# Kernel optimization log

Hardware: AMD Instinct MI355X
Metric: run time of the kernel (lower is better)

Reference implementation:

```python
import jax, jax.numpy as jnp
import numpy as np
from jax import lax

EPS = 1e-9

def _squash(v):
    # v: [..., D]; squash nonlinearity from CapsNet
    n = jnp.sum(jnp.square(v), axis=-1, keepdims=True)
    return (n / (1.0 + n) / jnp.sqrt(n + EPS)) * v

def setup_inputs() -> dict:
    key = jax.random.key(0)
    ks = jax.random.split(key, 12)
    B, S, D, NI = 1024, 200, 64, 4
    N_UID, N_MID = 50000, 100000
    return {
        "uid": jax.random.randint(ks[0], (B,), 0, N_UID, dtype=jnp.int32),
        "age": jax.random.randint(ks[1], (B,), 0, N_UID, dtype=jnp.int32),
        "gender": jax.random.randint(ks[2], (B,), 0, N_UID, dtype=jnp.int32),
        "occup": jax.random.randint(ks[3], (B,), 0, N_UID, dtype=jnp.int32),
        "mid_his": jax.random.randint(ks[4], (B, S), 0, N_MID, dtype=jnp.int32),
        "mask": jax.random.randint(ks[5], (B, S), 0, 2).astype(jnp.float32),
        "user_emb_table": jax.random.normal(ks[6], (N_UID, D), jnp.float32) * 0.1,
        "age_table": jax.random.normal(ks[7], (N_UID, D), jnp.float32) * 0.1,
        "gender_table": jax.random.normal(ks[8], (N_UID, D), jnp.float32) * 0.1,
        "occup_table": jax.random.normal(ks[9], (N_UID, D), jnp.float32) * 0.1,
        "mid_emb_table": jax.random.normal(ks[10], (N_MID, D), jnp.float32) * 0.1,
        "w_capsule": jax.random.normal(ks[11], (S, NI * D, D), jnp.float32),
    }

def reference(uid, age, gender, occup, mid_his, mask,
              user_emb_table, age_table, gender_table, occup_table,
              mid_emb_table, w_capsule):
    NI = 4
    B, S = mid_his.shape
    D = mid_emb_table.shape[1]

    # user profile: mean of 4 stacked user feature embeddings
    user_profile = (user_emb_table[uid] + gender_table[gender]
                    + age_table[age] + occup_table[occup]) * 0.25  # [B,D]

    # masked item history embeddings
    item_his = mid_emb_table[mid_his] * mask[:, :, None]  # [B,S,D]

    # adjacency: sigmoid(sum_d h_i[d]*h_j[d]*u[d]) without [B,S,S,D] blowup
    hu = item_his * user_profile[:, None, :]              # [B,S,D]
    adj = jax.nn.sigmoid(jnp.einsum('bid,bjd->bij', hu, item_his))  # [B,S,S]
    adj = adj * mask[:, None, :] * mask[:, :, None]

    # --- CapsuleNetwork, bilinear_type=2 ---
    # TF: sum(w[1,S,NI*D,D] * u[B,S,1,D], axis=3) == contraction over D
    hat = jnp.einsum('bsd,sed->bse', item_his, w_capsule)  # [B,S,NI*D]
    hat = hat.reshape(B, S, NI, D).transpose(0, 2, 1, 3)   # [B,NI,S,D]
    hat_iter = lax.stop_gradient(hat)

    cw = jnp.zeros((B, NI, S), dtype=item_his.dtype)  # routing logits
    atten_mask = mask[:, None, :]                     # [B,1,S] broadcast over NI
    for i in range(3):
        sw = jax.nn.softmax(cw, axis=1)               # softmax over interests
        sw = jnp.where(atten_mask == 0, 0.0, sw)      # [B,NI,S]
        if i < 2:
            cap = _squash(jnp.einsum('bks,bksd->bkd', sw, hat_iter))  # [B,NI,D]
            delta = jnp.einsum('bksd,bkd->bks', hat_iter, cap)
            cw = cw + delta
        else:
            cap = _squash(jnp.einsum('bks,bksd->bkd', sw, hat))
    interest_capsule = cap  # [B,NI,D]; relu_layer=False -> no projection
    return interest_capsule, adj
```

## Files before the change

### kernel.cpp

```cpp
#include <hip/hip_runtime.h>

#define B_SZ 1024
#define S_SZ 200
#define D_SZ 64
#define NI_SZ 4
#define E_SZ 256

using u16 = unsigned short;
using u32 = unsigned int;
typedef short  sh8    __attribute__((ext_vector_type(8)));
typedef __bf16 bf16x8 __attribute__((ext_vector_type(8)));
typedef float  f32x4  __attribute__((ext_vector_type(4)));

__device__ __forceinline__ u16 f2bf(float x) {
  u32 u = __float_as_uint(x);
  u += 0x7FFFu + ((u >> 16) & 1u);
  return (u16)(u >> 16);
}
__device__ __forceinline__ float bf2f(u16 h) {
  return __uint_as_float(((u32)h) << 16);
}
__device__ __forceinline__ sh8 ldsr(const u16* arr, int row, int kshort) {
  const int idx = row * 64 + (kshort ^ ((row & 7) << 3));
  return *(const sh8*)(arr + idx);
}
__device__ __forceinline__ bf16x8 ldsw(const u16* arr, int row, int kshort) {
  return __builtin_bit_cast(bf16x8, ldsr(arr, row, kshort));
}
__device__ __forceinline__ void stsw(u16* arr, int row, int c, sh8 v) {
  *(sh8*)(arr + row * 64 + 8 * (c ^ (row & 7))) = v;
}

__global__ __launch_bounds__(256) void wconv_kernel(
    const float* __restrict__ W, u16* __restrict__ Wb)
{
  const int idx = blockIdx.x * 256 + threadIdx.x;
  if (idx >= S_SZ * E_SZ * D_SZ / 8) return;
  const float4 a = *(const float4*)(W + (size_t)idx * 8);
  const float4 b = *(const float4*)(W + (size_t)idx * 8 + 4);
  sh8 r;
  r[0] = (short)f2bf(a.x); r[1] = (short)f2bf(a.y);
  r[2] = (short)f2bf(a.z); r[3] = (short)f2bf(a.w);
  r[4] = (short)f2bf(b.x); r[5] = (short)f2bf(b.y);
  r[6] = (short)f2bf(b.z); r[7] = (short)f2bf(b.w);
  *(sh8*)(Wb + (size_t)idx * 8) = r;
}

__global__ __launch_bounds__(256, 4) void adj_fused(
    const int* __restrict__ uid, const int* __restrict__ age,
    const int* __restrict__ gender, const int* __restrict__ occup,
    const float* __restrict__ U, const float* __restrict__ AT,
    const float* __restrict__ GT, const float* __restrict__ OT,
    const int* __restrict__ mid_his, const float* __restrict__ mask,
    const float* __restrict__ memb,
    u16* __restrict__ item_bs, float* __restrict__ adj)
{
  const int b = blockIdx.x;
  __shared__ u16   Hs[208 * 64];
  __shared__ float Ms[208];
  __shared__ int   midS[S_SZ];
  __shared__ float pS[D_SZ];
  const int tid = threadIdx.x;

  if (tid < 208) Ms[tid] = (tid < S_SZ) ? mask[b * S_SZ + tid] : 0.f;
  if (tid < S_SZ) midS[tid] = mid_his[b * S_SZ + tid];
  if (tid < D_SZ) {
    float v = U[(size_t)uid[b]    * D_SZ + tid]
            + GT[(size_t)gender[b] * D_SZ + tid]
            + AT[(size_t)age[b]    * D_SZ + tid]
            + OT[(size_t)occup[b]  * D_SZ + tid];
    pS[tid] = 0.25f * v;
  }
  __syncthreads();

  for (int idx = tid; idx < S_SZ * 8; idx += 256) {
    const int row = idx >> 3, c = idx & 7;
    const float m = Ms[row];
    const float* src = memb + (size_t)midS[row] * D_SZ + c * 8;
    const float4 a = *(const float4*)(src);
    const float4 d = *(const float4*)(src + 4);
    sh8 v;
    v[0] = (short)f2bf(a.x * m); v[1] = (short)f2bf(a.y * m);
    v[2] = (short)f2bf(a.z * m); v[3] = (short)f2bf(a.w * m);
    v[4] = (short)f2bf(d.x * m); v[5] = (short)f2bf(d.y * m);
    v[6] = (short)f2bf(d.z * m); v[7] = (short)f2bf(d.w * m);
    stsw(Hs, row, c, v);
    *(sh8*)(item_bs + ((size_t)b * S_SZ + row) * D_SZ + c * 8) = v;
  }
  if (tid < 64) {
    sh8 z = {0,0,0,0,0,0,0,0};
    stsw(Hs, S_SZ + (tid >> 3), tid & 7, z);
  }
  __syncthreads();

  const int w = tid >> 6, l = tid & 63;
  const int lr = l & 15, lg = l >> 4;
  float pvA[8], pvB[8];
  #pragma unroll
  for (int j = 0; j < 8; j++) { pvA[j] = pS[lg * 8 + j]; pvB[j] = pS[32 + lg * 8 + j]; }

  float* outb = adj + (size_t)b * S_SZ * S_SZ;
  for (int mt = 0; mt < 13; mt++) {
    const int arow = mt * 16 + lr;
    const sh8 r0 = ldsr(Hs, arow, lg * 8);
    const sh8 r1 = ldsr(Hs, arow, 32 + lg * 8);
    sh8 h0, h1;
    #pragma unroll
    for (int j = 0; j < 8; j++) {
      h0[j] = (short)f2bf(bf2f((u16)r0[j]) * pvA[j]);
      h1[j] = (short)f2bf(bf2f((u16)r1[j]) * pvB[j]);
    }
    const bf16x8 a0 = __builtin_bit_cast(bf16x8, h0);
    const bf16x8 a1 = __builtin_bit_cast(bf16x8, h1);
    for (int nt = w; nt < 13; nt += 4) {
      const int brow = nt * 16 + lr;
      const bf16x8 b0 = ldsw(Hs, brow, lg * 8);
      const bf16x8 b1 = ldsw(Hs, brow, 32 + lg * 8);
      f32x4 acc = {0.f, 0.f, 0.f, 0.f};
      acc = __builtin_amdgcn_mfma_f32_16x16x32_bf16(a0, b0, acc, 0, 0, 0);
      acc = __builtin_amdgcn_mfma_f32_16x16x32_bf16(a1, b1, acc, 0, 0, 0);
      const int n = nt * 16 + lr;
      const float mj = Ms[n];
      #pragma unroll
      for (int r = 0; r < 4; r++) {
        const int m = mt * 16 + lg * 4 + r;
        if (m < S_SZ && n < S_SZ) {
          const float sg = 1.f / (1.f + __expf(-acc[r]));
          outb[(size_t)m * S_SZ + n] = sg * Ms[m] * mj;
        }
      }
    }
  }
}

__global__ __launch_bounds__(256, 4) void hat_mfma(
    const u16* __restrict__ item_bs, const u16* __restrict__ Wb,
    u16* __restrict__ hatb)
{
  const int s  = blockIdx.y;
  const int b0 = blockIdx.x * 64;
  __shared__ u16 As[64 * 64];
  __shared__ u16 Ws_[256 * 64];
  const int tid = threadIdx.x;

  for (int idx = tid; idx < 64 * 8; idx += 256) {
    const int row = idx >> 3, c = idx & 7;
    const sh8 v = *(const sh8*)(item_bs + ((size_t)(b0 + row) * S_SZ + s) * D_SZ + c * 8);
    stsw(As, row, c, v);
  }
  for (int idx = tid; idx < 256 * 8; idx += 256) {
    const int row = idx >> 3, c = idx & 7;
    const sh8 v = *(const sh8*)(Wb + ((size_t)s * E_SZ + row) * D_SZ + c * 8);
    stsw(Ws_, row, c, v);
  }
  __syncthreads();

  const int w = tid >> 6, l = tid & 63;
  const int lr = l & 15, lg = l >> 4;

  f32x4 acc[4][4];
  #pragma unroll
  for (int mt = 0; mt < 4; mt++)
    #pragma unroll
    for (int nt = 0; nt < 4; nt++) acc[mt][nt] = (f32x4){0.f, 0.f, 0.f, 0.f};

  #pragma unroll
  for (int ks = 0; ks < 2; ks++) {
    bf16x8 af[4], bf_[4];
    #pragma unroll
    for (int mt = 0; mt < 4; mt++)
      af[mt] = ldsw(As, mt * 16 + lr, ks * 32 + lg * 8);
    #pragma unroll
    for (int nt = 0; nt < 4; nt++)
      bf_[nt] = ldsw(Ws_, w * 64 + nt * 16 + lr, ks * 32 + lg * 8);
    #pragma unroll
    for (int mt = 0; mt < 4; mt++)
      #pragma unroll
      for (int nt = 0; nt < 4; nt++)
        acc[mt][nt] = __builtin_amdgcn_mfma_f32_16x16x32_bf16(af[mt], bf_[nt], acc[mt][nt], 0, 0, 0);
  }

  #pragma unroll
  for (int mt = 0; mt < 4; mt++) {
    #pragma unroll
    for (int r = 0; r < 4; r++) {
      const int bb = b0 + mt * 16 + lg * 4 + r;
      u16* dst = hatb + (((size_t)bb * NI_SZ + w) * S_SZ + s) * D_SZ;
      #pragma unroll
      for (int nt = 0; nt < 4; nt++)
        dst[nt * 16 + lr] = f2bf(acc[mt][nt][r]);
    }
  }
}

__device__ __forceinline__ float rlane(float v, int l) {
  return __int_as_float(__builtin_amdgcn_readlane(__float_as_int(v), l));
}

__global__ __launch_bounds__(1024, 4) void route_kernel(
    const u16* __restrict__ hatb, const float* __restrict__ mask,
    float* __restrict__ out)
{
  const int b = blockIdx.x;
  const int t = threadIdx.x;
  const int w = t >> 6, lane = t & 63;
  const int k = w >> 2, q = w & 3;
  __shared__ float cwS[NI_SZ][212];
  __shared__ float partS[NI_SZ][4][D_SZ];

  const float msv = (lane < 50) ? mask[b * S_SZ + q * 50 + lane] : 0.f;

  float hr[50];
  const u16* hg = hatb + (((size_t)b * NI_SZ + k) * S_SZ + q * 50) * D_SZ + lane;
  #pragma unroll
  for (int j = 0; j < 50; j++) hr[j] = bf2f(hg[j * D_SZ]);
  #pragma unroll
  for (int j = 0; j < 50; j++) asm volatile("" : "+v"(hr[j]));

  const int jj = __brev(lane) >> 26;

  for (int iter = 0; iter < 3; ++iter) {
    float swv;
    if (iter == 0) {
      swv = 0.25f * msv;
    } else {
      const int sidx = q * 50 + (lane < 50 ? lane : 49);
      const float a0 = cwS[0][sidx], a1 = cwS[1][sidx],
                  a2 = cwS[2][sidx], a3 = cwS[3][sidx];
      const float mx = fmaxf(fmaxf(a0, a1), fmaxf(a2, a3));
      const float e0 = __expf(a0 - mx), e1 = __expf(a1 - mx),
                  e2 = __expf(a2 - mx), e3 = __expf(a3 - mx);
      const float ek = (k == 0) ? e0 : (k == 1) ? e1 : (k == 2) ? e2 : e3;
      const float inv = 1.f / (e0 + e1 + e2 + e3);
      swv = (msv == 0.f) ? 0.f : ek * inv;
    }

    float c0 = 0.f, c1 = 0.f, c2 = 0.f, c3 = 0.f;
    #pragma unroll
    for (int j = 0; j < 48; j += 4) {
      c0 = fmaf(rlane(swv, j + 0), hr[j + 0], c0);
      c1 = fmaf(rlane(swv, j + 1), hr[j + 1], c1);
      c2 = fmaf(rlane(swv, j + 2), hr[j + 2], c2);
      c3 = fmaf(rlane(swv, j + 3), hr[j + 3], c3);
    }
    c0 = fmaf(rlane(swv, 48), hr[48], c0);
    c1 = fmaf(rlane(swv, 49), hr[49], c1);
    partS[k][q][lane] = (c0 + c2) + (c1 + c3);
    __syncthreads();

    const float cap = partS[k][0][lane] + partS[k][1][lane]
                    + partS[k][2][lane] + partS[k][3][lane];
    float n = cap * cap;
    #pragma unroll
    for (int off = 32; off; off >>= 1) n += __shfl_xor(n, off);
    const float f = n / (1.f + n) * rsqrtf(n + 1e-9f);
    const float capd = cap * f;

    if (iter < 2) {
      float p[32];
      {
        const int bit = lane & 1;
        #pragma unroll
        for (int j = 0; j < 32; j++) {
          const float lo = hr[j] * capd;
          const float hi = (j + 32 < 50) ? hr[j + 32] * capd : 0.f;
          const float send = bit ? lo : hi;
          const float keep = bit ? hi : lo;
          p[j] = keep + __shfl_xor(send, 1);
        }
      }
      #pragma unroll
      for (int r = 1; r < 6; r++) {
        const int dist = 1 << r;
        const int half = 32 >> r;
        const int bit = (lane >> r) & 1;
        #pragma unroll
        for (int j = 0; j < 32; j++) {
          if (j < half) {
            const float send = bit ? p[j] : p[j + half];
            const float keep = bit ? p[j + half] : p[j];
            p[j] = keep + __shfl_xor(send, dist);
          }
        }
      }
      if (jj < 50) {
        if (iter == 0) cwS[k][q * 50 + jj] = p[0];
        else           cwS[k][q * 50 + jj] += p[0];
      }
      __syncthreads();
    } else if (q == 0) {
      out[((size_t)b * NI_SZ + k) * D_SZ + lane] = capd;
    }
  }
}

extern "C" void kernel_launch(void* const* d_in, const int* in_sizes, int n_in,
                              void* d_out, int out_size, void* d_ws, size_t ws_size,
                              hipStream_t stream)
{
  const int*   uid     = (const int*)d_in[0];
  const int*   age     = (const int*)d_in[1];
  const int*   gender  = (const int*)d_in[2];
  const int*   occup   = (const int*)d_in[3];
  const int*   mid_his = (const int*)d_in[4];
  const float* mask    = (const float*)d_in[5];
  const float* U       = (const float*)d_in[6];
  const float* AT      = (const float*)d_in[7];
  const float* GT      = (const float*)d_in[8];
  const float* OT      = (const float*)d_in[9];
  const float* ME      = (const float*)d_in[10];
  const float* WC      = (const float*)d_in[11];

  float* out  = (float*)d_out;
  float* adj  = out + B_SZ * NI_SZ * D_SZ;

  char* ws = (char*)d_ws;
  u16*   item_bs = (u16*)ws;
  u16*   Wb      = (u16*)(ws + 26214400);
  u16*   hatb    = (u16*)(ws + 26214400 + 6553600);

  wconv_kernel<<<(S_SZ * E_SZ * D_SZ / 8 + 255) / 256, 256, 0, stream>>>(WC, Wb);
  adj_fused<<<B_SZ, 256, 0, stream>>>(uid, age, gender, occup, U, AT, GT, OT,
                                      mid_his, mask, ME, item_bs, adj);
  hat_mfma<<<dim3(16, S_SZ), 256, 0, stream>>>(item_bs, Wb, hatb);
  route_kernel<<<B_SZ, 1024, 0, stream>>>(hatb, mask, out);
}
```

Measured before the change: 169.7 us.

## Merge adj, weight conversion and hat GEMM into one interleaved heterogeneous kernel

Replaces three launches (weight fp32→bf16 conversion, adjacency kernel, hat GEMM) with a single kernel whose blocks are split into adjacency blocks and hat-GEMM blocks, interleaved 8:25 per group. The hat blocks now gather item embeddings and convert W directly from fp32, so the item_bs and Wb workspace round trips and two launch boundaries go away. The cost is redundant fp32 W loads and conversions (each W slice is read by 16 blocks) and redundant embedding gathers, and the two work types must share one launch configuration and one shared-memory size.

Result: slower. 177.6 us (+4.6%).

```diff
diff --git a/kernel.cpp b/kernel.cpp
--- a/kernel.cpp
+++ b/kernel.cpp
@@ -30,165 +30,151 @@
 __device__ __forceinline__ void stsw(u16* arr, int row, int c, sh8 v) {
   *(sh8*)(arr + row * 64 + 8 * (c ^ (row & 7))) = v;
 }
-
-__global__ __launch_bounds__(256) void wconv_kernel(
-    const float* __restrict__ W, u16* __restrict__ Wb)
-{
-  const int idx = blockIdx.x * 256 + threadIdx.x;
-  if (idx >= S_SZ * E_SZ * D_SZ / 8) return;
-  const float4 a = *(const float4*)(W + (size_t)idx * 8);
-  const float4 b = *(const float4*)(W + (size_t)idx * 8 + 4);
-  sh8 r;
-  r[0] = (short)f2bf(a.x); r[1] = (short)f2bf(a.y);
-  r[2] = (short)f2bf(a.z); r[3] = (short)f2bf(a.w);
-  r[4] = (short)f2bf(b.x); r[5] = (short)f2bf(b.y);
-  r[6] = (short)f2bf(b.z); r[7] = (short)f2bf(b.w);
-  *(sh8*)(Wb + (size_t)idx * 8) = r;
-}
-
-__global__ __launch_bounds__(256, 4) void adj_fused(
+__device__ __forceinline__ sh8 cvt8(const float* __restrict__ src, float m) {
+  const float4 a = *(const float4*)(src);
+  const float4 d = *(const float4*)(src + 4);
+  sh8 v;
+  v[0] = (short)f2bf(a.x * m); v[1] = (short)f2bf(a.y * m);
+  v[2] = (short)f2bf(a.z * m); v[3] = (short)f2bf(a.w * m);
+  v[4] = (short)f2bf(d.x * m); v[5] = (short)f2bf(d.y * m);
+  v[6] = (short)f2bf(d.z * m); v[7] = (short)f2bf(d.w * m);
+  return v;
+}
+
+__global__ __launch_bounds__(256, 4) void mega_kernel(
     const int* __restrict__ uid, const int* __restrict__ age,
     const int* __restrict__ gender, const int* __restrict__ occup,
     const float* __restrict__ U, const float* __restrict__ AT,
     const float* __restrict__ GT, const float* __restrict__ OT,
     const int* __restrict__ mid_his, const float* __restrict__ mask,
-    const float* __restrict__ memb,
-    u16* __restrict__ item_bs, float* __restrict__ adj)
+    const float* __restrict__ memb, const float* __restrict__ WC,
+    float* __restrict__ adj, u16* __restrict__ hatb)
 {
-  const int b = blockIdx.x;
-  __shared__ u16   Hs[208 * 64];
-  __shared__ float Ms[208];
-  __shared__ int   midS[S_SZ];
-  __shared__ float pS[D_SZ];
+  __shared__ __align__(16) char smem[40960];
   const int tid = threadIdx.x;
-
-  if (tid < 208) Ms[tid] = (tid < S_SZ) ? mask[b * S_SZ + tid] : 0.f;
-  if (tid < S_SZ) midS[tid] = mid_his[b * S_SZ + tid];
-  if (tid < D_SZ) {
-    float v = U[(size_t)uid[b]    * D_SZ + tid]
-            + GT[(size_t)gender[b] * D_SZ + tid]
-            + AT[(size_t)age[b]    * D_SZ + tid]
-            + OT[(size_t)occup[b]  * D_SZ + tid];
-    pS[tid] = 0.25f * v;
-  }
-  __syncthreads();
-
-  for (int idx = tid; idx < S_SZ * 8; idx += 256) {
-    const int row = idx >> 3, c = idx & 7;
-    const float m = Ms[row];
-    const float* src = memb + (size_t)midS[row] * D_SZ + c * 8;
-    const float4 a = *(const float4*)(src);
-    const float4 d = *(const float4*)(src + 4);
-    sh8 v;
-    v[0] = (short)f2bf(a.x * m); v[1] = (short)f2bf(a.y * m);
-    v[2] = (short)f2bf(a.z * m); v[3] = (short)f2bf(a.w * m);
-    v[4] = (short)f2bf(d.x * m); v[5] = (short)f2bf(d.y * m);
-    v[6] = (short)f2bf(d.z * m); v[7] = (short)f2bf(d.w * m);
-    stsw(Hs, row, c, v);
-    *(sh8*)(item_bs + ((size_t)b * S_SZ + row) * D_SZ + c * 8) = v;
-  }
-  if (tid < 64) {
-    sh8 z = {0,0,0,0,0,0,0,0};
-    stsw(Hs, S_SZ + (tid >> 3), tid & 7, z);
-  }
-  __syncthreads();
-
-  const int w = tid >> 6, l = tid & 63;
-  const int lr = l & 15, lg = l >> 4;
-  float pvA[8], pvB[8];
-  #pragma unroll
-  for (int j = 0; j < 8; j++) { pvA[j] = pS[lg * 8 + j]; pvB[j] = pS[32 + lg * 8 + j]; }
-
-  float* outb = adj + (size_t)b * S_SZ * S_SZ;
-  for (int mt = 0; mt < 13; mt++) {
-    const int arow = mt * 16 + lr;
-    const sh8 r0 = ldsr(Hs, arow, lg * 8);
-    const sh8 r1 = ldsr(Hs, arow, 32 + lg * 8);
-    sh8 h0, h1;
-    #pragma unroll
-    for (int j = 0; j < 8; j++) {
-      h0[j] = (short)f2bf(bf2f((u16)r0[j]) * pvA[j]);
-      h1[j] = (short)f2bf(bf2f((u16)r1[j]) * pvB[j]);
-    }
-    const bf16x8 a0 = __builtin_bit_cast(bf16x8, h0);
-    const bf16x8 a1 = __builtin_bit_cast(bf16x8, h1);
-    for (int nt = w; nt < 13; nt += 4) {
-      const int brow = nt * 16 + lr;
-      const bf16x8 b0 = ldsw(Hs, brow, lg * 8);
-      const bf16x8 b1 = ldsw(Hs, brow, 32 + lg * 8);
-      f32x4 acc = {0.f, 0.f, 0.f, 0.f};
-      acc = __builtin_amdgcn_mfma_f32_16x16x32_bf16(a0, b0, acc, 0, 0, 0);
-      acc = __builtin_amdgcn_mfma_f32_16x16x32_bf16(a1, b1, acc, 0, 0, 0);
-      const int n = nt * 16 + lr;
-      const float mj = Ms[n];
-      #pragma unroll
-      for (int r = 0; r < 4; r++) {
-        const int m = mt * 16 + lg * 4 + r;
-        if (m < S_SZ && n < S_SZ) {
-          const float sg = 1.f / (1.f + __expf(-acc[r]));
-          outb[(size_t)m * S_SZ + n] = sg * Ms[m] * mj;
+  const int g = blockIdx.x / 33, r = blockIdx.x % 33;
+
+  if (r < 8) {
+    const int b = g * 8 + r;
+    u16*   Hs   = (u16*)smem;
+    float* Ms   = (float*)(smem + 26624);
+    int*   midS = (int*)(smem + 27456);
+    float* pS   = (float*)(smem + 28256);
+
+    if (tid < 208) Ms[tid] = (tid < S_SZ) ? mask[b * S_SZ + tid] : 0.f;
+    if (tid < S_SZ) midS[tid] = mid_his[b * S_SZ + tid];
+    if (tid < D_SZ) {
+      float v = U[(size_t)uid[b]     * D_SZ + tid]
+              + GT[(size_t)gender[b] * D_SZ + tid]
+              + AT[(size_t)age[b]    * D_SZ + tid]
+              + OT[(size_t)occup[b]  * D_SZ + tid];
+      pS[tid] = 0.25f * v;
+    }
+    __syncthreads();
+
+    for (int idx = tid; idx < S_SZ * 8; idx += 256) {
+      const int row = idx >> 3, c = idx & 7;
+      stsw(Hs, row, c, cvt8(memb + (size_t)midS[row] * D_SZ + c * 8, Ms[row]));
+    }
+    if (tid < 64) {
+      sh8 z = {0,0,0,0,0,0,0,0};
+      stsw(Hs, S_SZ + (tid >> 3), tid & 7, z);
+    }
+    __syncthreads();
+
+    const int w = tid >> 6, l = tid & 63;
+    const int lr = l & 15, lg = l >> 4;
+    float pvA[8], pvB[8];
+    #pragma unroll
+    for (int j = 0; j < 8; j++) { pvA[j] = pS[lg * 8 + j]; pvB[j] = pS[32 + lg * 8 + j]; }
+
+    float* outb = adj + (size_t)b * S_SZ * S_SZ;
+    for (int mt = 0; mt < 13; mt++) {
+      const int arow = mt * 16 + lr;
+      const sh8 r0 = ldsr(Hs, arow, lg * 8);
+      const sh8 r1 = ldsr(Hs, arow, 32 + lg * 8);
+      sh8 h0, h1;
+      #pragma unroll
+      for (int j = 0; j < 8; j++) {
+        h0[j] = (short)f2bf(bf2f((u16)r0[j]) * pvA[j]);
+        h1[j] = (short)f2bf(bf2f((u16)r1[j]) * pvB[j]);
+      }
+      const bf16x8 a0 = __builtin_bit_cast(bf16x8, h0);
+      const bf16x8 a1 = __builtin_bit_cast(bf16x8, h1);
+      for (int nt = w; nt < 13; nt += 4) {
+        const int brow = nt * 16 + lr;
+        const bf16x8 b0 = ldsw(Hs, brow, lg * 8);
+        const bf16x8 b1 = ldsw(Hs, brow, 32 + lg * 8);
+        f32x4 acc = {0.f, 0.f, 0.f, 0.f};
+        acc = __builtin_amdgcn_mfma_f32_16x16x32_bf16(a0, b0, acc, 0, 0, 0);
+        acc = __builtin_amdgcn_mfma_f32_16x16x32_bf16(a1, b1, acc, 0, 0, 0);
+        const int n = nt * 16 + lr;
+        const float mj = Ms[n];
+        #pragma unroll
+        for (int rr = 0; rr < 4; rr++) {
+          const int m = mt * 16 + lg * 4 + rr;
+          if (m < S_SZ && n < S_SZ) {
+            const float sg = 1.f / (1.f + __expf(-acc[rr]));
+            outb[(size_t)m * S_SZ + n] = sg * Ms[m] * mj;
+          }
         }
       }
     }
-  }
-}
-
-__global__ __launch_bounds__(256, 4) void hat_mfma(
-    const u16* __restrict__ item_bs, const u16* __restrict__ Wb,
-    u16* __restrict__ hatb)
-{
-  const int s  = blockIdx.y;
-  const int b0 = blockIdx.x * 64;
-  __shared__ u16 As[64 * 64];
-  __shared__ u16 Ws_[256 * 64];
-  const int tid = threadIdx.x;
-
-  for (int idx = tid; idx < 64 * 8; idx += 256) {
-    const int row = idx >> 3, c = idx & 7;
-    const sh8 v = *(const sh8*)(item_bs + ((size_t)(b0 + row) * S_SZ + s) * D_SZ + c * 8);
-    stsw(As, row, c, v);
-  }
-  for (int idx = tid; idx < 256 * 8; idx += 256) {
-    const int row = idx >> 3, c = idx & 7;
-    const sh8 v = *(const sh8*)(Wb + ((size_t)s * E_SZ + row) * D_SZ + c * 8);
-    stsw(Ws_, row, c, v);
-  }
-  __syncthreads();
-
-  const int w = tid >> 6, l = tid & 63;
-  const int lr = l & 15, lg = l >> 4;
-
-  f32x4 acc[4][4];
-  #pragma unroll
-  for (int mt = 0; mt < 4; mt++)
-    #pragma unroll
-    for (int nt = 0; nt < 4; nt++) acc[mt][nt] = (f32x4){0.f, 0.f, 0.f, 0.f};
-
-  #pragma unroll
-  for (int ks = 0; ks < 2; ks++) {
-    bf16x8 af[4], bf_[4];
+  } else {
+    const int hi = g * 25 + (r - 8);
+    const int s  = hi >> 4;
+    const int b0 = (hi & 15) * 64;
+    u16* As  = (u16*)smem;
+    u16* Ws_ = (u16*)(smem + 8192);
+
+    for (int idx = tid; idx < 64 * 8; idx += 256) {
+      const int row = idx >> 3, c = idx & 7;
+      const int bb = b0 + row;
+      const int mid = mid_his[bb * S_SZ + s];
+      const float m = mask[bb * S_SZ + s];
+      stsw(As, row, c, cvt8(memb + (size_t)mid * D_SZ + c * 8, m));
+    }
+    for (int idx = tid; idx < 256 * 8; idx += 256) {
+      const int row = idx >> 3, c = idx & 7;
+      stsw(Ws_, row, c, cvt8(WC + ((size_t)s * E_SZ + row) * D_SZ + c * 8, 1.f));
+    }
+    __syncthreads();
+
+    const int w = tid >> 6, l = tid & 63;
+    const int lr = l & 15, lg = l >> 4;
+
+    f32x4 acc[4][4];
     #pragma unroll
     for (int mt = 0; mt < 4; mt++)
-      af[mt] = ldsw(As, mt * 16 + lr, ks * 32 + lg * 8);
-    #pragma unroll
-    for (int nt = 0; nt < 4; nt++)
-      bf_[nt] = ldsw(Ws_, w * 64 + nt * 16 + lr, ks * 32 + lg * 8);
-    #pragma unroll
-    for (int mt = 0; mt < 4; mt++)
+      #pragma unroll
+      for (int nt = 0; nt < 4; nt++) acc[mt][nt] = (f32x4){0.f, 0.f, 0.f, 0.f};
+
+    #pragma unroll
+    for (int ks = 0; ks < 2; ks++) {
+      bf16x8 af[4], bf_[4];
+      #pragma unroll
+      for (int mt = 0; mt < 4; mt++)
+        af[mt] = ldsw(As, mt * 16 + lr, ks * 32 + lg * 8);
       #pragma unroll
       for (int nt = 0; nt < 4; nt++)
-        acc[mt][nt] = __builtin_amdgcn_mfma_f32_16x16x32_bf16(af[mt], bf_[nt], acc[mt][nt], 0, 0, 0);
-  }
-
-  #pragma unroll
-  for (int mt = 0; mt < 4; mt++) {
-    #pragma unroll
-    for (int r = 0; r < 4; r++) {
-      const int bb = b0 + mt * 16 + lg * 4 + r;
-      u16* dst = hatb + (((size_t)bb * NI_SZ + w) * S_SZ + s) * D_SZ;
-      #pragma unroll
-      for (int nt = 0; nt < 4; nt++)
-        dst[nt * 16 + lr] = f2bf(acc[mt][nt][r]);
+        bf_[nt] = ldsw(Ws_, w * 64 + nt * 16 + lr, ks * 32 + lg * 8);
+      #pragma unroll
+      for (int mt = 0; mt < 4; mt++)
+        #pragma unroll
+        for (int nt = 0; nt < 4; nt++)
+          acc[mt][nt] = __builtin_amdgcn_mfma_f32_16x16x32_bf16(af[mt], bf_[nt], acc[mt][nt], 0, 0, 0);
+    }
+
+    #pragma unroll
+    for (int mt = 0; mt < 4; mt++) {
+      #pragma unroll
+      for (int rr = 0; rr < 4; rr++) {
+        const int bb = b0 + mt * 16 + lg * 4 + rr;
+        u16* dst = hatb + (((size_t)bb * NI_SZ + w) * S_SZ + s) * D_SZ;
+        #pragma unroll
+        for (int nt = 0; nt < 4; nt++)
+          dst[nt * 16 + lr] = f2bf(acc[mt][nt][rr]);
+      }
     }
   }
 }
@@ -270,10 +256,10 @@
         }
       }
       #pragma unroll
-      for (int r = 1; r < 6; r++) {
-        const int dist = 1 << r;
-        const int half = 32 >> r;
-        const int bit = (lane >> r) & 1;
+      for (int rr = 1; rr < 6; rr++) {
+        const int dist = 1 << rr;
+        const int half = 32 >> rr;
+        const int bit = (lane >> rr) & 1;
         #pragma unroll
         for (int j = 0; j < 32; j++) {
           if (j < half) {
@@ -314,14 +300,9 @@
   float* out  = (float*)d_out;
   float* adj  = out + B_SZ * NI_SZ * D_SZ;
 
-  char* ws = (char*)d_ws;
-  u16*   item_bs = (u16*)ws;
-  u16*   Wb      = (u16*)(ws + 26214400);
-  u16*   hatb    = (u16*)(ws + 26214400 + 6553600);
-
-  wconv_kernel<<<(S_SZ * E_SZ * D_SZ / 8 + 255) / 256, 256, 0, stream>>>(WC, Wb);
-  adj_fused<<<B_SZ, 256, 0, stream>>>(uid, age, gender, occup, U, AT, GT, OT,
-                                      mid_his, mask, ME, item_bs, adj);
-  hat_mfma<<<dim3(16, S_SZ), 256, 0, stream>>>(item_bs, Wb, hatb);
+  u16* hatb = (u16*)d_ws;
+
+  mega_kernel<<<4224, 256, 0, stream>>>(uid, age, gender, occup, U, AT, GT, OT,
+                                        mid_his, mask, ME, WC, adj, hatb);
   route_kernel<<<B_SZ, 1024, 0, stream>>>(hatb, mask, out);
 }
```
